# Optimization experiments

Hardware: AMD Instinct MI355X
Metric: run time of the kernel (lower is better)

## Reference

```python
import jax, jax.numpy as jnp
import numpy as np

N, C, K, P, Q, PS = 32, 128, 128, 64, 64, 3

def setup_inputs() -> dict:
    key = jax.random.key(0)
    k1, k2, k3 = jax.random.split(key, 3)
    x = jax.random.normal(k1, (N, C, P, Q), dtype=jnp.float32)
    W = jax.random.normal(k2, (K, C * PS * PS), dtype=jnp.float32) * (1.0 / np.sqrt(C * PS * PS))
    perturbs = jax.random.normal(k3, (N, K, P, Q), dtype=jnp.float32)
    return {"x": x, "W": W, "perturbs": perturbs}

def reference(x, W, perturbs):
    # patchify (pad=1, unfold 3x3, stride 1) + matmul with W^T is exactly a
    # 3x3 SAME convolution: flatten order of patchify is (C, kh, kw), matching
    # conv.weight.reshape(k, -1). Express it as a direct conv (no im2col blowup).
    k = W.shape[0]
    c = x.shape[1]
    w = W.reshape(k, c, PS, PS)  # OIHW
    out = jax.lax.conv_general_dilated(
        x, w,
        window_strides=(1, 1),
        padding=((1, 1), (1, 1)),
        dimension_numbers=("NCHW", "OIHW", "NCHW"),
    )
    return out + perturbs
```

## Files before the change

### kernel.cpp

```cpp
#include <hip/hip_runtime.h>
#include <hip/hip_bf16.h>

#define NN 32
#define CCH 128
#define KK 128
#define PP 64
#define QQ 64

typedef __bf16 bf16x8 __attribute__((ext_vector_type(8)));
typedef float f32x16 __attribute__((ext_vector_type(16)));
typedef float f32x4 __attribute__((ext_vector_type(4)));

#define XT_ELEMS (32ull * 64 * 64 * 128)

__global__ __launch_bounds__(256) void prep_x(const float* __restrict__ x,
                                              __bf16* __restrict__ xT) {
    __shared__ float tile[128 * 64];
    const int t = threadIdx.x;
    const int p = blockIdx.x;
    const int n = blockIdx.y;

#pragma unroll
    for (int pass = 0; pass < 8; ++pass) {
        int idx = pass * 256 + t;
        int qf = idx & 15;
        int c  = idx >> 4;
        f32x4 v = *(const f32x4*)(x + (((size_t)n * CCH + c) * PP + p) * QQ + qf * 4);
        int key = ((c >> 3) & 15) * 4;
        *(f32x4*)(tile + c * 64 + ((qf * 4) ^ key)) = v;
    }
    __syncthreads();

#pragma unroll
    for (int pass = 0; pass < 4; ++pass) {
        int cc   = pass * 2 + (t >> 7);
        int rem  = t & 127;
        int q    = rem >> 1;
        int half = rem & 1;
        int c0   = cc * 16 + half * 8;
        int key  = ((c0 >> 3) & 15) * 4;
        bf16x8 o;
#pragma unroll
        for (int j = 0; j < 8; ++j) o[j] = (__bf16)tile[(c0 + j) * 64 + (q ^ key)];
        *(bf16x8*)(xT + ((((size_t)n * 8 + cc) * PP + p) * QQ + q) * 16 + half * 8) = o;
    }
}

__global__ __launch_bounds__(256) void prep_w(const float* __restrict__ W,
                                              __bf16* __restrict__ Wf) {
    const int id = blockIdx.x * 256 + threadIdx.x;
    const int lane = id & 63;
    const int r1   = id >> 6;
    const int kb   = r1 & 3;
    const int r2   = r1 >> 2;
    const int t    = r2 % 9;
    const int cc   = r2 / 9;

    const int k  = kb * 32 + (lane & 31);
    const int c0 = cc * 16 + (lane >> 5) * 8;

    bf16x8 o;
#pragma unroll
    for (int j = 0; j < 8; ++j)
        o[j] = (__bf16)W[(size_t)k * (CCH * 9) + (size_t)(c0 + j) * 9 + t];
    ((bf16x8*)Wf)[id] = o;
}

#define XPITCH 2112
#define WBYTES 36864
#define XROWS  10
#define XBYTES (XROWS * XPITCH)

__global__ __launch_bounds__(512, 2) void conv_main(const __bf16* __restrict__ xT,
                                                    const __bf16* __restrict__ Wf,
                                                    const float* __restrict__ per,
                                                    float* __restrict__ out) {
    __shared__ __align__(16) char wlds[2][WBYTES];
    __shared__ __align__(16) char xlds[2][XBYTES];

    const int tid  = threadIdx.x;
    const int lane = tid & 63;
    const int w    = tid >> 6;
    const int kbs  = w & 1;
    const int pb   = w >> 1;
    const int n    = blockIdx.y;
    const int p0   = blockIdx.x * 8;
    const int m    = lane & 31;
    const int half = lane >> 5;

    if (tid < 40) {
        int row = tid >> 2, part = tid & 3;
        int off = row * XPITCH + (part >> 1) * 2080 + (part & 1) * 16;
        *(f32x4*)(xlds[0] + off) = f32x4{0.f, 0.f, 0.f, 0.f};
        *(f32x4*)(xlds[1] + off) = f32x4{0.f, 0.f, 0.f, 0.f};
    }

    f32x16 acc[2][2][2];
#pragma unroll
    for (int a = 0; a < 2; ++a)
#pragma unroll
        for (int b = 0; b < 2; ++b)
#pragma unroll
            for (int c = 0; c < 2; ++c)
#pragma unroll
                for (int e = 0; e < 16; ++e) acc[a][b][c][e] = 0.f;

    const char* xb = (const char*)xT + ((size_t)n * 8) * PP * QQ * 32;

    auto stage = [&](int ccn, int buf) {
        const char* g = (const char*)Wf + (size_t)ccn * WBYTES;
#pragma unroll
        for (int it = 0; it < 5; ++it) {
            int idx = it * 512 + tid;
            if (idx < WBYTES / 16) {
                __builtin_amdgcn_global_load_lds(
                    (const __attribute__((address_space(1))) unsigned int*)(g + idx * 16),
                    (__attribute__((address_space(3))) unsigned int*)(wlds[buf] + idx * 16),
                    16, 0, 0);
            }
        }
        const char* gx = xb + (size_t)ccn * (PP * QQ * 32);
#pragma unroll
        for (int it = 0; it < 3; ++it) {
            int gi = it * 512 + tid;
            if (gi < XROWS * 128) {
                int row = gi >> 7;
                int wi  = (gi & 127) * 16;
                int r   = p0 - 1 + row;
                int rc  = r < 0 ? 0 : (r > 63 ? 63 : r);
                __builtin_amdgcn_global_load_lds(
                    (const __attribute__((address_space(1))) unsigned int*)(gx + (size_t)rc * 2048 + wi),
                    (__attribute__((address_space(3))) unsigned int*)(xlds[buf] + row * XPITCH + 32 + wi),
                    16, 0, 0);
            }
        }
    };

    auto compute = [&](int buf) {
        const char* wbase = wlds[buf];
        const char* xbase = xlds[buf];

        bf16x8 a_cur[3][2], a_prev[3][2];
#pragma unroll
        for (int ri = 0; ri < 4; ++ri) {
            const int rr = pb * 2 + ri;
            const int r  = p0 + pb * 2 + ri - 1;
            const bool rok = ((unsigned)r < (unsigned)PP);

            bf16x8 b[3][2];
            if (rok) {
                const char* rbase = xbase + rr * XPITCH + half * 16;
#pragma unroll
                for (int dq = 0; dq < 3; ++dq)
#pragma unroll
                    for (int qb = 0; qb < 2; ++qb)
                        b[dq][qb] = *(const bf16x8*)(rbase + (qb * 32 + m + dq) * 32);
            }

            if (ri < 3) {
#pragma unroll
                for (int dq = 0; dq < 3; ++dq)
#pragma unroll
                    for (int kb = 0; kb < 2; ++kb)
                        a_cur[dq][kb] = ((const bf16x8*)wbase)[((ri * 3 + dq) * 4 +
                                                                kbs * 2 + kb) * 64 + lane];
            }

            if (rok) {
                if (ri >= 1) {
#pragma unroll
                    for (int dq = 0; dq < 3; ++dq)
#pragma unroll
                        for (int kb = 0; kb < 2; ++kb)
#pragma unroll
                            for (int qb = 0; qb < 2; ++qb)
                                acc[1][kb][qb] = __builtin_amdgcn_mfma_f32_32x32x16_bf16(
                                    a_prev[dq][kb], b[dq][qb], acc[1][kb][qb], 0, 0, 0);
                }
                if (ri < 3) {
#pragma unroll
                    for (int dq = 0; dq < 3; ++dq)
#pragma unroll
                        for (int kb = 0; kb < 2; ++kb)
#pragma unroll
                            for (int qb = 0; qb < 2; ++qb)
                                acc[0][kb][qb] = __builtin_amdgcn_mfma_f32_32x32x16_bf16(
                                    a_cur[dq][kb], b[dq][qb], acc[0][kb][qb], 0, 0, 0);
                }
            }

            if (ri < 3) {
#pragma unroll
                for (int dq = 0; dq < 3; ++dq)
#pragma unroll
                    for (int kb = 0; kb < 2; ++kb) a_prev[dq][kb] = a_cur[dq][kb];
            }
        }
    };

    stage(0, 0);
    __syncthreads();

    for (int cc = 0; cc < 7; ++cc) {
        stage(cc + 1, (cc + 1) & 1);
        compute(cc & 1);
        __syncthreads();
    }

    auto tile_addr = [&](int it, int j) -> size_t {
        int oi = it >> 2, kbi = (it >> 1) & 1, qb = it & 1;
        int prow = p0 + pb * 2 + oi;
        int k = (kbs * 2 + kbi) * 32 + (lane >> 3) + j * 8;
        int q = qb * 32 + (lane & 7) * 4;
        return (((size_t)n * KK + k) * PP + prow) * QQ + q;
    };

    float* scr = (float*)(wlds[0] + w * 4096);

    auto process = [&](int it, f32x4 (&pv)[4]) {
        int oi = it >> 2, kbi = (it >> 1) & 1, qb = it & 1;
        f32x16 v = acc[oi][kbi][qb];
#pragma unroll
        for (int r = 0; r < 16; ++r) {
            int kl = (r & 3) + 8 * (r >> 2) + 4 * half;
            scr[kl * 32 + ((((m >> 2) ^ (kl & 7)) << 2) | (m & 3))] = v[r];
        }
#pragma unroll
        for (int j = 0; j < 4; ++j) {
            int kl = (lane >> 3) + j * 8;
            f32x4 d = *(const f32x4*)(scr + kl * 32 + (((lane & 7) ^ (kl & 7)) << 2));
            f32x4 s = d + pv[j];
            __builtin_nontemporal_store(s, (f32x4*)(out + tile_addr(it, j)));
        }
    };

    f32x4 pv0[4], pv1[4];
#pragma unroll
    for (int j = 0; j < 4; ++j) pv0[j] = *(const f32x4*)(per + tile_addr(0, j));

    compute(1);

#pragma unroll
    for (int itp = 0; itp < 4; ++itp) {
        const int itA = itp * 2, itB = itp * 2 + 1;
#pragma unroll
        for (int j = 0; j < 4; ++j) pv1[j] = *(const f32x4*)(per + tile_addr(itB, j));
        process(itA, pv0);
        if (itp < 3) {
#pragma unroll
            for (int j = 0; j < 4; ++j)
                pv0[j] = *(const f32x4*)(per + tile_addr(itA + 2, j));
        }
        process(itB, pv1);
    }
}

extern "C" void kernel_launch(void* const* d_in, const int* in_sizes, int n_in,
                              void* d_out, int out_size, void* d_ws, size_t ws_size,
                              hipStream_t stream) {
    const float* x   = (const float*)d_in[0];
    const float* W   = (const float*)d_in[1];
    const float* per = (const float*)d_in[2];
    float* out = (float*)d_out;

    __bf16* xT = (__bf16*)d_ws;
    __bf16* Wf = (__bf16*)((char*)d_ws + XT_ELEMS * 2);

    prep_x<<<dim3(PP, NN), 256, 0, stream>>>(x, xT);
    prep_w<<<dim3(72), 256, 0, stream>>>(W, Wf);
    conv_main<<<dim3(PP / 8, NN), 512, 0, stream>>>(xT, Wf, per, out);
}
```

Baseline: 211.5 us.

## Load conv weights directly from global and halve rows per block

Weights are no longer staged into LDS; each wave reads its A fragments straight from global memory (relying on L2/L1 caching). The block shrinks to 256 threads covering 4 output rows, doubling the grid and cutting LDS use to a small x tile plus a dedicated epilogue scratch area. This removes the weight-staging traffic and LDS pressure, allowing more blocks per CU. In exchange, global-load latency now sits directly in the MFMA loop and the x halo is re-read more often per output row.

After: 209.6 us. About the same (-0.9%).

```diff
diff --git a/kernel.cpp b/kernel.cpp
--- a/kernel.cpp
+++ b/kernel.cpp
@@ -67,16 +67,15 @@
 }
 
 #define XPITCH 2112
-#define WBYTES 36864
-#define XROWS  10
+#define XROWS  6
 #define XBYTES (XROWS * XPITCH)
 
-__global__ __launch_bounds__(512, 2) void conv_main(const __bf16* __restrict__ xT,
+__global__ __launch_bounds__(256, 2) void conv_main(const __bf16* __restrict__ xT,
                                                     const __bf16* __restrict__ Wf,
                                                     const float* __restrict__ per,
                                                     float* __restrict__ out) {
-    __shared__ __align__(16) char wlds[2][WBYTES];
     __shared__ __align__(16) char xlds[2][XBYTES];
+    __shared__ __align__(16) char scr_lds[4][4096];
 
     const int tid  = threadIdx.x;
     const int lane = tid & 63;
@@ -84,11 +83,11 @@
     const int kbs  = w & 1;
     const int pb   = w >> 1;
     const int n    = blockIdx.y;
-    const int p0   = blockIdx.x * 8;
+    const int p0   = blockIdx.x * 4;
     const int m    = lane & 31;
     const int half = lane >> 5;
 
-    if (tid < 40) {
+    if (tid < 24) {
         int row = tid >> 2, part = tid & 3;
         int off = row * XPITCH + (part >> 1) * 2080 + (part & 1) * 16;
         *(f32x4*)(xlds[0] + off) = f32x4{0.f, 0.f, 0.f, 0.f};
@@ -107,38 +106,27 @@
 
     const char* xb = (const char*)xT + ((size_t)n * 8) * PP * QQ * 32;
 
-    auto stage = [&](int ccn, int buf) {
-        const char* g = (const char*)Wf + (size_t)ccn * WBYTES;
-#pragma unroll
-        for (int it = 0; it < 5; ++it) {
-            int idx = it * 512 + tid;
-            if (idx < WBYTES / 16) {
-                __builtin_amdgcn_global_load_lds(
-                    (const __attribute__((address_space(1))) unsigned int*)(g + idx * 16),
-                    (__attribute__((address_space(3))) unsigned int*)(wlds[buf] + idx * 16),
-                    16, 0, 0);
-            }
-        }
+    const bf16x8* wg = (const bf16x8*)Wf + kbs * 128 + lane;
+
+    auto stage_x = [&](int ccn, int buf) {
         const char* gx = xb + (size_t)ccn * (PP * QQ * 32);
 #pragma unroll
         for (int it = 0; it < 3; ++it) {
-            int gi = it * 512 + tid;
-            if (gi < XROWS * 128) {
-                int row = gi >> 7;
-                int wi  = (gi & 127) * 16;
-                int r   = p0 - 1 + row;
-                int rc  = r < 0 ? 0 : (r > 63 ? 63 : r);
-                __builtin_amdgcn_global_load_lds(
-                    (const __attribute__((address_space(1))) unsigned int*)(gx + (size_t)rc * 2048 + wi),
-                    (__attribute__((address_space(3))) unsigned int*)(xlds[buf] + row * XPITCH + 32 + wi),
-                    16, 0, 0);
-            }
-        }
-    };
-
-    auto compute = [&](int buf) {
-        const char* wbase = wlds[buf];
+            int gi  = it * 256 + tid;
+            int row = gi >> 7;
+            int wi  = (gi & 127) * 16;
+            int r   = p0 - 1 + row;
+            int rc  = r < 0 ? 0 : (r > 63 ? 63 : r);
+            __builtin_amdgcn_global_load_lds(
+                (const __attribute__((address_space(1))) unsigned int*)(gx + (size_t)rc * 2048 + wi),
+                (__attribute__((address_space(3))) unsigned int*)(xlds[buf] + row * XPITCH + 32 + wi),
+                16, 0, 0);
+        }
+    };
+
+    auto compute = [&](int buf, int cc) {
         const char* xbase = xlds[buf];
+        const bf16x8* wc = wg + (size_t)cc * 2304;
 
         bf16x8 a_cur[3][2], a_prev[3][2];
 #pragma unroll
@@ -162,8 +150,7 @@
                 for (int dq = 0; dq < 3; ++dq)
 #pragma unroll
                     for (int kb = 0; kb < 2; ++kb)
-                        a_cur[dq][kb] = ((const bf16x8*)wbase)[((ri * 3 + dq) * 4 +
-                                                                kbs * 2 + kb) * 64 + lane];
+                        a_cur[dq][kb] = wc[((ri * 3 + dq) * 4 + kb) * 64];
             }
 
             if (rok) {
@@ -198,12 +185,12 @@
         }
     };
 
-    stage(0, 0);
+    stage_x(0, 0);
     __syncthreads();
 
     for (int cc = 0; cc < 7; ++cc) {
-        stage(cc + 1, (cc + 1) & 1);
-        compute(cc & 1);
+        stage_x(cc + 1, (cc + 1) & 1);
+        compute(cc & 1, cc);
         __syncthreads();
     }
 
@@ -215,7 +202,7 @@
         return (((size_t)n * KK + k) * PP + prow) * QQ + q;
     };
 
-    float* scr = (float*)(wlds[0] + w * 4096);
+    float* scr = (float*)scr_lds[w];
 
     auto process = [&](int it, f32x4 (&pv)[4]) {
         int oi = it >> 2, kbi = (it >> 1) & 1, qb = it & 1;
@@ -238,7 +225,7 @@
 #pragma unroll
     for (int j = 0; j < 4; ++j) pv0[j] = *(const f32x4*)(per + tile_addr(0, j));
 
-    compute(1);
+    compute(1, 7);
 
 #pragma unroll
     for (int itp = 0; itp < 4; ++itp) {
@@ -268,5 +255,5 @@
 
     prep_x<<<dim3(PP, NN), 256, 0, stream>>>(x, xT);
     prep_w<<<dim3(72), 256, 0, stream>>>(W, Wf);
-    conv_main<<<dim3(PP / 8, NN), 512, 0, stream>>>(xT, Wf, per, out);
-}
+    conv_main<<<dim3(PP / 4, NN), 256, 0, stream>>>(xT, Wf, per, out);
+}
```
